# Kernel tuning notes

Hardware: AMD Instinct MI355X
Metric: run time of the kernel (lower is better)

Reference implementation:

```python
import jax, jax.numpy as jnp
import numpy as np

EPS = 1e-5

def gelu(x):
    return jax.nn.gelu(x, approximate=False)

def conv1x1(x, w, b):
    # x: [B,C,H,W], w: [O,C], b: [O]
    return jnp.einsum('bchw,oc->bohw', x, w) + b[None, :, None, None]

def dwconv3(x, w, b):
    # depthwise 3x3, w: [C,1,3,3]
    C = x.shape[1]
    y = jax.lax.conv_general_dilated(x, w, (1, 1), 'SAME',
                                     feature_group_count=C,
                                     dimension_numbers=('NCHW', 'OIHW', 'NCHW'))
    return y + b[None, :, None, None]

def groupnorm(x, g, b):
    # GroupNorm(1, C): normalize over (C,H,W) per sample, per-channel affine
    m = x.mean(axis=(1, 2, 3), keepdims=True)
    v = x.var(axis=(1, 2, 3), keepdims=True)
    xn = (x - m) * jax.lax.rsqrt(v + EPS)
    return xn * g[None, :, None, None] + b[None, :, None, None]

@jax.custom_vjp
def spike(u):
    return (u > 0.0).astype(u.dtype)

def _spike_fwd(u):
    return spike(u), u

def _spike_bwd(u, g):
    # rectangular surrogate gradient of width 0.5 around the threshold
    return (g * (jnp.abs(u) < 0.5).astype(g.dtype),)

spike.defvjp(_spike_fwd, _spike_bwd)

def lif_along(x, tau, vth, axis):
    # leaky-integrate-fire recurrence along `axis` (H or W) treated as time
    xt = jnp.moveaxis(x, axis, 0)  # [T, ...]
    z = jnp.zeros_like(xt[0])
    def step(carry, x_t):
        u_prev, o_prev = carry
        u = x_t + tau * u_prev * (1.0 - o_prev)  # hard reset on spike
        o = spike(u - vth)
        return (u, o), o
    _, out = jax.lax.scan(step, (z, z), xt)
    return jnp.moveaxis(out, 0, axis)


def setup_inputs() -> dict:
    key = jax.random.key(0)
    ks = jax.random.split(key, 8)
    B, C, H, W = 64, 96, 56, 56
    Hd = 4 * C
    def w(k, shape, s=0.02):
        return jax.random.normal(k, shape, jnp.float32) * s
    f32 = jnp.float32
    return dict(
        x=jax.random.normal(ks[0], (B, C, H, W), f32),
        n1g=jnp.ones(C, f32), n1b=jnp.zeros(C, f32),
        c1w=w(ks[1], (C, C)), c1b=jnp.zeros(C, f32),
        g1g=jnp.ones(C, f32), g1b=jnp.zeros(C, f32),
        dww=w(ks[2], (C, 1, 3, 3)), dwb=jnp.zeros(C, f32),
        g2g=jnp.ones(C, f32), g2b=jnp.zeros(C, f32),
        tau1=jnp.array(0.25, f32), vth1=jnp.array(-1.0, f32),
        tau2=jnp.array(0.25, f32), vth2=jnp.array(-1.0, f32),
        c21w=w(ks[3], (C, C)), c21b=jnp.zeros(C, f32),
        c22w=w(ks[4], (C, C)), c22b=jnp.zeros(C, f32),
        g3g=jnp.ones(C, f32), g3b=jnp.zeros(C, f32),
        c3w=w(ks[5], (C, C)), c3b=jnp.zeros(C, f32),
        n2g=jnp.ones(C, f32), n2b=jnp.zeros(C, f32),
        f1w=w(ks[6], (Hd, C)), f1b=jnp.zeros(Hd, f32),
        f2w=w(ks[7], (C, Hd)), f2b=jnp.zeros(C, f32),
    )


def reference(x, n1g, n1b, c1w, c1b, g1g, g1b, dww, dwb, g2g, g2b,
              tau1, vth1, tau2, vth2, c21w, c21b, c22w, c22b,
              g3g, g3b, c3w, c3b, n2g, n2b, f1w, f1b, f2w, f2b):
    shortcut = x
    # LIF module
    h = groupnorm(x, n1g, n1b)                               # block norm1 (MyNorm)
    h = gelu(groupnorm(conv1x1(h, c1w, c1b), g1g, g1b))      # conv1 -> norm1 -> GELU
    h = gelu(groupnorm(dwconv3(h, dww, dwb), g2g, g2b))      # dw1 -> norm2 -> GELU
    x_lr = lif_along(h, tau1, vth1, axis=2)                  # LIF over H
    x_td = lif_along(h, tau2, vth2, axis=3)                  # LIF over W
    h = gelu(conv1x1(x_lr, c21w, c21b)) + gelu(conv1x1(x_td, c22w, c22b))
    h = conv1x1(groupnorm(h, g3g, g3b), c3w, c3b)            # norm3 -> conv3
    x = shortcut + h
    # MLP branch (1x1 convs)
    m = groupnorm(x, n2g, n2b)
    m = conv1x1(gelu(conv1x1(m, f1w, f1b)), f2w, f2b)
    return x + m
```

## Files before the change

### kernel.cpp

```cpp
#include <hip/hip_runtime.h>

#define BB 64
#define CC 96
#define HH 56
#define WW 56
#define HWSZ (HH*WW)
#define CHW (CC*HWSZ)
#define NTOT ((size_t)BB*CHW)
#define S_SPLIT 32
#define CHUNK (CHW/S_SPLIT)
#define HD 384
#define NP 104

typedef float f32x4  __attribute__((ext_vector_type(4)));
typedef short bf16x8 __attribute__((ext_vector_type(8)));
typedef unsigned short u16x4 __attribute__((ext_vector_type(4)));

__device__ __forceinline__ unsigned short f2bf(float f) {
    unsigned int u = __float_as_uint(f);
    u = (u + 0x7FFFu + ((u >> 16) & 1u)) >> 16;
    return (unsigned short)u;
}
__device__ __forceinline__ unsigned int cvtpk(float lo, float hi) {
    unsigned int r;
    asm("v_cvt_pk_bf16_f32 %0, %1, %2" : "=v"(r) : "v"(lo), "v"(hi));
    return r;
}
__device__ __forceinline__ unsigned short cvt1(float x) {
    return (unsigned short)cvtpk(x, x);
}
__device__ __forceinline__ float bf2f(unsigned short u) {
    return __uint_as_float(((unsigned int)u) << 16);
}
__device__ __forceinline__ float gelu_t(float x) {
    float s = x*x;
    float q = __builtin_fmaf(s, 0.102943f, 2.3021953f) * x;
    float t = exp2f(q);
    float r = __builtin_amdgcn_rcpf(1.0f + t);
    return __builtin_fmaf(-x, r, x);
}
__device__ __forceinline__ bf16x8 ldfrag(const unsigned short* p) {
    return *reinterpret_cast<const bf16x8*>(p);
}
template<int NPART>
__device__ __forceinline__ float2 stats_from_parts(const float2* __restrict__ part, int b) {
    int lane = threadIdx.x & 63;
    float s = 0.f, q = 0.f;
    for (int i = lane; i < NPART; i += 64) {
        float2 v = part[b*NPART + i];
        s += v.x; q += v.y;
    }
    #pragma unroll
    for (int off = 32; off > 0; off >>= 1) {
        s += __shfl_down(s, off);
        q += __shfl_down(q, off);
    }
    s = __shfl(s, 0); q = __shfl(q, 0);
    float mean = s / (float)CHW;
    float var  = q / (float)CHW - mean*mean;
    return make_float2(mean, rsqrtf(var + 1e-5f));
}

__global__ __launch_bounds__(256) void wconv(const float* __restrict__ c1w, const float* __restrict__ c21w,
        const float* __restrict__ c22w, const float* __restrict__ c3w,
        const float* __restrict__ f1w, const float* __restrict__ f2w,
        unsigned short* __restrict__ wbf) {
    int i = blockIdx.x*256 + threadIdx.x;
    int blk = i / 9216;
    int idx = i - blk*9216;
    int tm   = idx / 1536;
    int rem  = idx - tm*1536;
    int ks   = rem / 512;
    int rem2 = rem - ks*512;
    int lane = rem2 >> 3;
    int j    = rem2 & 7;
    int row = tm*16 + (lane & 15);
    int col = ks*32 + (lane >> 4)*8 + j;
    float v;
    if      (blk == 0) v = c1w [row*CC + col];
    else if (blk == 1) v = c21w[row*CC + col];
    else if (blk == 2) v = c22w[row*CC + col];
    else if (blk == 3) v = c3w [row*CC + col];
    else if (blk <  8) v = f1w[((blk-4)*CC + row)*CC + col];
    else               v = f2w[row*HD + (blk-8)*CC + col];
    wbf[i] = f2bf(v);
}

__global__ __launch_bounds__(256) void gn_partial(const float* __restrict__ in, float2* __restrict__ part) {
    int b = blockIdx.y, s = blockIdx.x;
    const float4* p = (const float4*)(in + (size_t)b*CHW + (size_t)s*CHUNK);
    float sum = 0.f, sq = 0.f;
    for (int i = threadIdx.x; i < CHUNK/4; i += 256) {
        float4 v = p[i];
        sum += v.x+v.y+v.z+v.w;
        sq  += v.x*v.x+v.y*v.y+v.z*v.z+v.w*v.w;
    }
    #pragma unroll
    for (int off = 32; off > 0; off >>= 1) {
        sum += __shfl_down(sum, off);
        sq  += __shfl_down(sq,  off);
    }
    __shared__ float2 red[4];
    int wid = threadIdx.x >> 6, lane = threadIdx.x & 63;
    if (lane == 0) red[wid] = make_float2(sum, sq);
    __syncthreads();
    if (threadIdx.x == 0) {
        for (int i = 1; i < 4; i++) { sum += red[i].x; sq += red[i].y; }
        part[b*S_SPLIT + s] = make_float2(sum, sq);
    }
}

template<bool IN_BF, bool OUT_RES, int NPART>
__global__ __launch_bounds__(256) void convk(const void* __restrict__ in_,
        const unsigned short* __restrict__ wbf, const float* __restrict__ bias,
        const float2* __restrict__ part_in, const float* __restrict__ gam, const float* __restrict__ bet,
        const float* __restrict__ res, void* __restrict__ out_, float2* __restrict__ part_out) {
    __shared__ unsigned short xs[128][NP];
    __shared__ float af0[CC], bf0[CC], af1[CC], bf1[CC];
    __shared__ float2 red[4];
    int tid = threadIdx.x;
    int b0 = blockIdx.y, b1 = b0 + 32;
    int hw0 = blockIdx.x * 64;
    int lane = tid & 63, wv = tid >> 6;
    int mh = wv >> 1, cg = wv & 1;
    bf16x8 wfr[9];
    {
        const unsigned short* wl = wbf + mh*4608 + lane*8;
        #pragma unroll
        for (int i = 0; i < 9; i++) wfr[i] = ldfrag(wl + i*512);
    }
    float2 st0 = stats_from_parts<NPART>(part_in, b0);
    float2 st1 = stats_from_parts<NPART>(part_in, b1);
    if (tid < CC) {
        float a0 = st0.y * gam[tid];
        af0[tid] = a0; bf0[tid] = __builtin_fmaf(-st0.x, a0, bet[tid]);
        float a1 = st1.y * gam[tid];
        af1[tid] = a1; bf1[tid] = __builtin_fmaf(-st1.x, a1, bet[tid]);
    }
    __syncthreads();
    if (IN_BF) {
        const unsigned short* inb = (const unsigned short*)in_;
        int colp = (tid & 31) * 2;
        for (int c4 = (tid >> 5)*4; c4 < CC; c4 += 32) {
            float v0[4][2], v1[4][2];
            #pragma unroll
            for (int j = 0; j < 4; j++) {
                int c = c4 + j;
                unsigned int u0 = *reinterpret_cast<const unsigned int*>(inb + (size_t)b0*CHW + (size_t)c*HWSZ + hw0 + colp);
                unsigned int u1 = *reinterpret_cast<const unsigned int*>(inb + (size_t)b1*CHW + (size_t)c*HWSZ + hw0 + colp);
                v0[j][0] = __builtin_fmaf(bf2f((unsigned short)u0),        af0[c], bf0[c]);
                v0[j][1] = __builtin_fmaf(bf2f((unsigned short)(u0>>16)),  af0[c], bf0[c]);
                v1[j][0] = __builtin_fmaf(bf2f((unsigned short)u1),        af1[c], bf1[c]);
                v1[j][1] = __builtin_fmaf(bf2f((unsigned short)(u1>>16)),  af1[c], bf1[c]);
            }
            *reinterpret_cast<uint2*>(&xs[colp][c4])      = make_uint2(cvtpk(v0[0][0],v0[1][0]), cvtpk(v0[2][0],v0[3][0]));
            *reinterpret_cast<uint2*>(&xs[colp+1][c4])    = make_uint2(cvtpk(v0[0][1],v0[1][1]), cvtpk(v0[2][1],v0[3][1]));
            *reinterpret_cast<uint2*>(&xs[64+colp][c4])   = make_uint2(cvtpk(v1[0][0],v1[1][0]), cvtpk(v1[2][0],v1[3][0]));
            *reinterpret_cast<uint2*>(&xs[64+colp+1][c4]) = make_uint2(cvtpk(v1[0][1],v1[1][1]), cvtpk(v1[2][1],v1[3][1]));
        }
    } else {
        int col = tid & 63;
        for (int c4 = (tid >> 6)*4; c4 < CC; c4 += 16) {
            float v0[4], v1[4];
            #pragma unroll
            for (int j = 0; j < 4; j++) {
                int c = c4 + j;
                size_t off0 = (size_t)b0*CHW + (size_t)c*HWSZ + hw0 + col;
                size_t off1 = (size_t)b1*CHW + (size_t)c*HWSZ + hw0 + col;
                float r0 = ((const float*)in_)[off0];
                float r1 = ((const float*)in_)[off1];
                v0[j] = __builtin_fmaf(r0, af0[c], bf0[c]);
                v1[j] = __builtin_fmaf(r1, af1[c], bf1[c]);
            }
            *reinterpret_cast<uint2*>(&xs[col][c4])    = make_uint2(cvtpk(v0[0],v0[1]), cvtpk(v0[2],v0[3]));
            *reinterpret_cast<uint2*>(&xs[64+col][c4]) = make_uint2(cvtpk(v1[0],v1[1]), cvtpk(v1[2],v1[3]));
        }
    }
    __syncthreads();
    int ln = lane & 15, k0 = (lane >> 4)*8, r0i = (lane >> 4)*4;
    f32x4 acc[3][4];
    #pragma unroll
    for (int t = 0; t < 3; t++)
        #pragma unroll
        for (int x = 0; x < 4; x++) acc[t][x] = (f32x4){0,0,0,0};
    __builtin_amdgcn_s_setprio(1);
    #pragma unroll
    for (int ks = 0; ks < 3; ks++) {
        bf16x8 bfr[4];
        #pragma unroll
        for (int xr = 0; xr < 4; xr++) bfr[xr] = ldfrag(&xs[cg*64 + xr*16 + ln][ks*32+k0]);
        #pragma unroll
        for (int tm = 0; tm < 3; tm++) {
            #pragma unroll
            for (int xr = 0; xr < 4; xr++)
                acc[tm][xr] = __builtin_amdgcn_mfma_f32_16x16x32_bf16(wfr[tm*3+ks], bfr[xr], acc[tm][xr], 0, 0, 0);
        }
    }
    __builtin_amdgcn_s_setprio(0);
    size_t obase = (size_t)(cg ? b1 : b0)*CHW + hw0;
    float s = 0.f, q = 0.f;
    #pragma unroll
    for (int tm = 0; tm < 3; tm++) {
        #pragma unroll
        for (int xr = 0; xr < 4; xr++) {
            #pragma unroll
            for (int r = 0; r < 4; r++) {
                int o = mh*48 + tm*16 + r0i + r;
                size_t idx = obase + (size_t)o*HWSZ + xr*16 + ln;
                float v = acc[tm][xr][r] + bias[o];
                if (OUT_RES) { v += res[idx]; ((float*)out_)[idx] = v; }
                else         { ((unsigned short*)out_)[idx] = cvt1(v); }
                s += v; q += v*v;
            }
        }
    }
    #pragma unroll
    for (int off = 32; off > 0; off >>= 1) { s += __shfl_down(s, off); q += __shfl_down(q, off); }
    if (lane == 0) red[wv] = make_float2(s, q);
    __syncthreads();
    if (tid == 0) {
        part_out[b0*49 + blockIdx.x] = make_float2(red[0].x + red[2].x, red[0].y + red[2].y);
        part_out[b1*49 + blockIdx.x] = make_float2(red[1].x + red[3].x, red[1].y + red[3].y);
    }
}

__global__ __launch_bounds__(256) void dw_fused(const unsigned short* __restrict__ t1,
        const float* __restrict__ dww, const float* __restrict__ dwb,
        const float2* __restrict__ part_in, const float* __restrict__ gam, const float* __restrict__ bet,
        unsigned short* __restrict__ t2, float2* __restrict__ part_out) {
    __shared__ float tile[HH*57];
    __shared__ float2 red[4];
    int bc = blockIdx.x;
    int b = bc / CC, c = bc - b*CC;
    int tid = threadIdx.x;
    float2 st = stats_from_parts<49>(part_in, b);
    float ga = gam[c]*st.y;
    float bb = __builtin_fmaf(-st.x, ga, bet[c]);
    const unsigned short* ip = t1 + (size_t)bc*HWSZ;
    for (int i = tid; i < HWSZ/4; i += 256) {
        u16x4 v = *reinterpret_cast<const u16x4*>(ip + (size_t)i*4);
        int h = i / 14;
        int w0 = (i - h*14)*4;
        float* tp = &tile[h*57 + w0];
        #pragma unroll
        for (int j = 0; j < 4; j++)
            tp[j] = gelu_t(__builtin_fmaf(bf2f((unsigned short)v[j]), ga, bb));
    }
    __syncthreads();
    float w00=dww[c*9+0],w01=dww[c*9+1],w02=dww[c*9+2],
          w10=dww[c*9+3],w11=dww[c*9+4],w12=dww[c*9+5],
          w20=dww[c*9+6],w21=dww[c*9+7],w22=dww[c*9+8];
    float bs = dwb[c];
    unsigned short* op = t2 + (size_t)bc*HWSZ;
    float s = 0.f, q = 0.f;
    for (int i = tid; i < HWSZ; i += 256) {
        int h = i/WW, w_ = i - h*WW;
        float acc = bs;
        int up = h > 0, dn = h < HH-1, lf = w_ > 0, rt = w_ < WW-1;
        const float* rm = &tile[(h-1)*57 + w_];
        const float* r0p = &tile[h*57 + w_];
        const float* rp = &tile[(h+1)*57 + w_];
        if (up) { if (lf) acc += rm[-1]*w00; acc += rm[0]*w01; if (rt) acc += rm[1]*w02; }
        if (lf) acc += r0p[-1]*w10;
        acc += r0p[0]*w11;
        if (rt) acc += r0p[1]*w12;
        if (dn) { if (lf) acc += rp[-1]*w20; acc += rp[0]*w21; if (rt) acc += rp[1]*w22; }
        op[i] = cvt1(acc);
        s += acc; q += acc*acc;
    }
    #pragma unroll
    for (int off = 32; off > 0; off >>= 1) { s += __shfl_down(s, off); q += __shfl_down(q, off); }
    int wid = tid >> 6, lane = tid & 63;
    if (lane == 0) red[wid] = make_float2(s, q);
    __syncthreads();
    if (tid == 0) {
        for (int i = 1; i < 4; i++) { s += red[i].x; q += red[i].y; }
        part_out[bc] = make_float2(s, q);
    }
}

__global__ __launch_bounds__(64) void lif_hw(const unsigned short* __restrict__ t2,
        unsigned short* __restrict__ xlr, unsigned short* __restrict__ xtd,
        const float2* __restrict__ part_in, const float* __restrict__ gam, const float* __restrict__ bet,
        const float* __restrict__ tau1p, const float* __restrict__ vth1p,
        const float* __restrict__ tau2p, const float* __restrict__ vth2p) {
    __shared__ unsigned short tile[HH*58];
    int bc = blockIdx.x;
    int b = bc / CC, c = bc - b*CC;
    int tid = threadIdx.x;
    float2 st = stats_from_parts<96>(part_in, b);
    float ga = gam[c]*st.y;
    float bb = __builtin_fmaf(-st.x, ga, bet[c]);
    const unsigned short* ip = t2 + (size_t)bc*HWSZ;
    for (int i = tid; i < HWSZ/4; i += 64) {
        u16x4 v = *reinterpret_cast<const u16x4*>(ip + i*4);
        int h = i / 14;
        int w0 = (i - h*14)*4;
        unsigned short* tp = &tile[h*58 + w0];
        #pragma unroll
        for (int j = 0; j < 4; j++)
            tp[j] = cvt1(gelu_t(__builtin_fmaf(bf2f((unsigned short)v[j]), ga, bb)));
    }
    __syncthreads();
    const float tau1 = *tau1p, vth1 = *vth1p;
    if (tid < WW) {
        float u = 0.f, o = 0.f;
        unsigned short* op = xlr + (size_t)bc*HWSZ + tid;
        for (int h = 0; h < HH; h++) {
            float xv = bf2f(tile[h*58 + tid]);
            u = xv + tau1*u*(1.f - o);
            o = (u - vth1 > 0.f) ? 1.f : 0.f;
            op[h*WW] = (o != 0.f) ? (unsigned short)0x3F80 : (unsigned short)0;
        }
    }
    __syncthreads();
    const float tau2 = *tau2p, vth2 = *vth2p;
    if (tid < HH) {
        float u = 0.f, o = 0.f;
        int off = tid*58;
        for (int w_ = 0; w_ < WW; w_++) {
            float xv = bf2f(tile[off + w_]);
            u = xv + tau2*u*(1.f - o);
            o = (u - vth2 > 0.f) ? 1.f : 0.f;
            tile[off + w_] = (o != 0.f) ? (unsigned short)0x3F80 : (unsigned short)0;
        }
    }
    __syncthreads();
    unsigned int* op32 = (unsigned int*)(xtd + (size_t)bc*HWSZ);
    for (int i = tid; i < HWSZ/2; i += 64) {
        int h = i / 28;
        int w0 = (i - h*28)*2;
        op32[i] = (unsigned int)tile[h*58 + w0] | ((unsigned int)tile[h*58 + w0 + 1] << 16);
    }
}

__global__ __launch_bounds__(256) void dual_mfma(const unsigned short* __restrict__ xa_g, const unsigned short* __restrict__ xb_g,
        const unsigned short* __restrict__ w1bf, const float* __restrict__ b1,
        const unsigned short* __restrict__ w2bf, const float* __restrict__ b2,
        unsigned short* __restrict__ out, float2* __restrict__ part_out) {
    __shared__ unsigned short xa[64][NP];
    __shared__ unsigned short xb[64][NP];
    __shared__ float2 red[4];
    int tid = threadIdx.x;
    int b = blockIdx.y;
    int hw0 = blockIdx.x * 64;
    {
        int colp = (tid & 31) * 2;
        const unsigned short* ap = xa_g + (size_t)b*CHW + hw0 + colp;
        const unsigned short* bp = xb_g + (size_t)b*CHW + hw0 + colp;
        for (int c4 = (tid >> 5)*4; c4 < CC; c4 += 32) {
            unsigned int ua[4], ub[4];
            #pragma unroll
            for (int j = 0; j < 4; j++) {
                ua[j] = *reinterpret_cast<const unsigned int*>(ap + (size_t)(c4+j)*HWSZ);
                ub[j] = *reinterpret_cast<const unsigned int*>(bp + (size_t)(c4+j)*HWSZ);
            }
            *reinterpret_cast<uint2*>(&xa[colp][c4]) =
                make_uint2((ua[0]&0xFFFFu)|(ua[1]<<16), (ua[2]&0xFFFFu)|(ua[3]<<16));
            *reinterpret_cast<uint2*>(&xa[colp+1][c4]) =
                make_uint2((ua[0]>>16)|(ua[1]&0xFFFF0000u), (ua[2]>>16)|(ua[3]&0xFFFF0000u));
            *reinterpret_cast<uint2*>(&xb[colp][c4]) =
                make_uint2((ub[0]&0xFFFFu)|(ub[1]<<16), (ub[2]&0xFFFFu)|(ub[3]<<16));
            *reinterpret_cast<uint2*>(&xb[colp+1][c4]) =
                make_uint2((ub[0]>>16)|(ub[1]&0xFFFF0000u), (ub[2]>>16)|(ub[3]&0xFFFF0000u));
        }
    }
    __syncthreads();
    int lane = tid & 63, wv = tid >> 6;
    int mh = wv >> 1, cg = wv & 1;
    int ln = lane & 15, k0 = (lane >> 4)*8, r0i = (lane >> 4)*4;
    const unsigned short* wl1 = w1bf + mh*4608 + lane*8;
    const unsigned short* wl2 = w2bf + mh*4608 + lane*8;
    f32x4 acc1[3][2], acc2[3][2];
    #pragma unroll
    for (int t = 0; t < 3; t++) {
        acc1[t][0] = (f32x4){0,0,0,0}; acc1[t][1] = (f32x4){0,0,0,0};
        acc2[t][0] = (f32x4){0,0,0,0}; acc2[t][1] = (f32x4){0,0,0,0};
    }
    __builtin_amdgcn_s_setprio(1);
    #pragma unroll
    for (int ks = 0; ks < 3; ks++) {
        bf16x8 bfa0 = ldfrag(&xa[cg*32 + ln][ks*32+k0]);
        bf16x8 bfa1 = ldfrag(&xa[cg*32 + 16 + ln][ks*32+k0]);
        bf16x8 bfb0 = ldfrag(&xb[cg*32 + ln][ks*32+k0]);
        bf16x8 bfb1 = ldfrag(&xb[cg*32 + 16 + ln][ks*32+k0]);
        #pragma unroll
        for (int tm = 0; tm < 3; tm++) {
            bf16x8 af1 = ldfrag(wl1 + (tm*3+ks)*512);
            bf16x8 af2 = ldfrag(wl2 + (tm*3+ks)*512);
            acc1[tm][0] = __builtin_amdgcn_mfma_f32_16x16x32_bf16(af1, bfa0, acc1[tm][0], 0, 0, 0);
            acc1[tm][1] = __builtin_amdgcn_mfma_f32_16x16x32_bf16(af1, bfa1, acc1[tm][1], 0, 0, 0);
            acc2[tm][0] = __builtin_amdgcn_mfma_f32_16x16x32_bf16(af2, bfb0, acc2[tm][0], 0, 0, 0);
            acc2[tm][1] = __builtin_amdgcn_mfma_f32_16x16x32_bf16(af2, bfb1, acc2[tm][1], 0, 0, 0);
        }
    }
    __builtin_amdgcn_s_setprio(0);
    size_t ob = (size_t)b*CHW + hw0;
    float s = 0.f, q = 0.f;
    #pragma unroll
    for (int tm = 0; tm < 3; tm++) {
        #pragma unroll
        for (int xr = 0; xr < 2; xr++) {
            #pragma unroll
            for (int r = 0; r < 4; r++) {
                int o = mh*48 + tm*16 + r0i + r;
                float v = gelu_t(acc1[tm][xr][r] + b1[o]) + gelu_t(acc2[tm][xr][r] + b2[o]);
                out[ob + (size_t)o*HWSZ + cg*32 + xr*16 + ln] = cvt1(v);
                s += v; q += v*v;
            }
        }
    }
    #pragma unroll
    for (int off = 32; off > 0; off >>= 1) { s += __shfl_down(s, off); q += __shfl_down(q, off); }
    if (lane == 0) red[wv] = make_float2(s, q);
    __syncthreads();
    if (tid == 0) {
        for (int i = 1; i < 4; i++) { s += red[i].x; q += red[i].y; }
        part_out[b*49 + blockIdx.x] = make_float2(s, q);
    }
}

__global__ __launch_bounds__(512, 4) void mlp_mfma(float* __restrict__ xio, const float2* __restrict__ part_in,
        const float* __restrict__ gam, const float* __restrict__ bet,
        const unsigned short* __restrict__ wbf, const float* __restrict__ b1, const float* __restrict__ b2) {
    __shared__ unsigned short xs[128][NP];
    __shared__ unsigned short mc[128][NP];
    __shared__ float afc[2][CC], bfc[2][CC];
    int tid = threadIdx.x;
    int b0 = blockIdx.y, b1i = b0 + 32;
    int hw0 = blockIdx.x * 64;
    int lane = tid & 63, wv = tid >> 6;
    int mh = wv >> 2;
    int cg = wv & 3;
    float2 st0 = stats_from_parts<49>(part_in, b0);
    float2 st1 = stats_from_parts<49>(part_in, b1i);
    if (tid < CC) {
        float a0 = st0.y * gam[tid];
        afc[0][tid] = a0; bfc[0][tid] = __builtin_fmaf(-st0.x, a0, bet[tid]);
        float a1 = st1.y * gam[tid];
        afc[1][tid] = a1; bfc[1][tid] = __builtin_fmaf(-st1.x, a1, bet[tid]);
    }
    __syncthreads();
    {
        int col = tid & 63;
        int bsel0 = (tid >> 6) & 1;
        size_t base = (size_t)(bsel0 ? b1i : b0)*CHW + hw0 + col;
        for (int c4 = (tid >> 7)*4; c4 < CC; c4 += 16) {
            float v[4];
            #pragma unroll
            for (int j = 0; j < 4; j++) {
                int c = c4 + j;
                float rv = xio[base + (size_t)c*HWSZ];
                v[j] = __builtin_fmaf(rv, afc[bsel0][c], bfc[bsel0][c]);
            }
            *reinterpret_cast<uint2*>(&xs[bsel0*64 + col][c4]) =
                make_uint2(cvtpk(v[0],v[1]), cvtpk(v[2],v[3]));
        }
    }
    __syncthreads();
    int ln = lane & 15, k0 = (lane >> 4)*8;
    int r0i = (lane >> 4)*4;
    int xrow0 = cg*32 + ln;
    int xrow1 = xrow0 + 16;
    int bsel = cg >> 1;
    size_t ob = (size_t)(bsel ? b1i : b0)*CHW + hw0 + (cg & 1)*32 + ln;
    float xv0[3][4], xv1[3][4];
    #pragma unroll
    for (int tm = 0; tm < 3; tm++) {
        #pragma unroll
        for (int r = 0; r < 4; r++) {
            size_t i0 = ob + (size_t)(mh*48 + tm*16 + r0i + r)*HWSZ;
            xv0[tm][r] = xio[i0];
            xv1[tm][r] = xio[i0 + 16];
        }
    }
    f32x4 ao[3][2];
    #pragma unroll
    for (int t = 0; t < 3; t++) { ao[t][0] = (f32x4){0,0,0,0}; ao[t][1] = (f32x4){0,0,0,0}; }
    for (int ch = 0; ch < 4; ch++) {
        const unsigned short* w1l = wbf + (4+ch)*9216 + mh*4608 + lane*8;
        const unsigned short* w2l = wbf + (8+ch)*9216 + mh*4608 + lane*8;
        f32x4 c1[3][2];
        #pragma unroll
        for (int t = 0; t < 3; t++) { c1[t][0] = (f32x4){0,0,0,0}; c1[t][1] = (f32x4){0,0,0,0}; }
        __builtin_amdgcn_s_setprio(1);
        #pragma unroll
        for (int ks = 0; ks < 3; ks++) {
            bf16x8 bfa = ldfrag(&xs[xrow0][ks*32+k0]);
            bf16x8 bfb = ldfrag(&xs[xrow1][ks*32+k0]);
            #pragma unroll
            for (int tm = 0; tm < 3; tm++) {
                bf16x8 af = ldfrag(w1l + (tm*3+ks)*512);
                c1[tm][0] = __builtin_amdgcn_mfma_f32_16x16x32_bf16(af, bfa, c1[tm][0], 0, 0, 0);
                c1[tm][1] = __builtin_amdgcn_mfma_f32_16x16x32_bf16(af, bfb, c1[tm][1], 0, 0, 0);
            }
        }
        __builtin_amdgcn_s_setprio(0);
        #pragma unroll
        for (int tm = 0; tm < 3; tm++) {
            int d0 = mh*48 + tm*16 + r0i;
            int dch = ch*CC + d0;
            float g0 = gelu_t(c1[tm][0][0] + b1[dch+0]);
            float g1 = gelu_t(c1[tm][0][1] + b1[dch+1]);
            float g2 = gelu_t(c1[tm][0][2] + b1[dch+2]);
            float g3 = gelu_t(c1[tm][0][3] + b1[dch+3]);
            *reinterpret_cast<uint2*>(&mc[xrow0][d0]) = make_uint2(cvtpk(g0,g1), cvtpk(g2,g3));
            float h0 = gelu_t(c1[tm][1][0] + b1[dch+0]);
            float h1 = gelu_t(c1[tm][1][1] + b1[dch+1]);
            float h2 = gelu_t(c1[tm][1][2] + b1[dch+2]);
            float h3 = gelu_t(c1[tm][1][3] + b1[dch+3]);
            *reinterpret_cast<uint2*>(&mc[xrow1][d0]) = make_uint2(cvtpk(h0,h1), cvtpk(h2,h3));
        }
        __syncthreads();
        __builtin_amdgcn_s_setprio(1);
        #pragma unroll
        for (int ks = 0; ks < 3; ks++) {
            bf16x8 bfa = ldfrag(&mc[xrow0][ks*32+k0]);
            bf16x8 bfb = ldfrag(&mc[xrow1][ks*32+k0]);
            #pragma unroll
            for (int tm = 0; tm < 3; tm++) {
                bf16x8 af = ldfrag(w2l + (tm*3+ks)*512);
                ao[tm][0] = __builtin_amdgcn_mfma_f32_16x16x32_bf16(af, bfa, ao[tm][0], 0, 0, 0);
                ao[tm][1] = __builtin_amdgcn_mfma_f32_16x16x32_bf16(af, bfb, ao[tm][1], 0, 0, 0);
            }
        }
        __builtin_amdgcn_s_setprio(0);
        __syncthreads();
    }
    #pragma unroll
    for (int tm = 0; tm < 3; tm++) {
        #pragma unroll
        for (int r = 0; r < 4; r++) {
            int o = mh*48 + tm*16 + r0i + r;
            size_t i0 = ob + (size_t)o*HWSZ;
            float bo = b2[o];
            xio[i0]      = xv0[tm][r] + bo + ao[tm][0][r];
            xio[i0 + 16] = xv1[tm][r] + bo + ao[tm][1][r];
        }
    }
}

extern "C" void kernel_launch(void* const* d_in, const int* in_sizes, int n_in,
                              void* d_out, int out_size, void* d_ws, size_t ws_size,
                              hipStream_t stream) {
    (void)in_sizes; (void)n_in; (void)out_size; (void)ws_size;
    const float* x    = (const float*)d_in[0];
    const float* n1g  = (const float*)d_in[1];
    const float* n1b  = (const float*)d_in[2];
    const float* c1w  = (const float*)d_in[3];
    const float* c1b  = (const float*)d_in[4];
    const float* g1g  = (const float*)d_in[5];
    const float* g1b  = (const float*)d_in[6];
    const float* dww  = (const float*)d_in[7];
    const float* dwb  = (const float*)d_in[8];
    const float* g2g  = (const float*)d_in[9];
    const float* g2b  = (const float*)d_in[10];
    const float* tau1 = (const float*)d_in[11];
    const float* vth1 = (const float*)d_in[12];
    const float* tau2 = (const float*)d_in[13];
    const float* vth2 = (const float*)d_in[14];
    const float* c21w = (const float*)d_in[15];
    const float* c21b = (const float*)d_in[16];
    const float* c22w = (const float*)d_in[17];
    const float* c22b = (const float*)d_in[18];
    const float* g3g  = (const float*)d_in[19];
    const float* g3b  = (const float*)d_in[20];
    const float* c3w  = (const float*)d_in[21];
    const float* c3b  = (const float*)d_in[22];
    const float* n2g  = (const float*)d_in[23];
    const float* n2b  = (const float*)d_in[24];
    const float* f1w  = (const float*)d_in[25];
    const float* f1b  = (const float*)d_in[26];
    const float* f2w  = (const float*)d_in[27];
    const float* f2b  = (const float*)d_in[28];
    float* out = (float*)d_out;

    unsigned short* A   = (unsigned short*)d_ws;
    unsigned short* Bb  = A  + NTOT;
    unsigned short* Cc  = Bb + NTOT;
    unsigned short* WBF = Cc + NTOT;
    float2* part0 = (float2*)(WBF + 110592);
    float2* part1 = part0 + 64*32;
    float2* part2 = part1 + 64*49;
    float2* part3 = part2 + 64*96;
    float2* part4 = part3 + 64*49;

    const unsigned short* Wc1  = WBF;
    const unsigned short* Wc21 = WBF + 9216;
    const unsigned short* Wc22 = WBF + 18432;
    const unsigned short* Wc3  = WBF + 27648;

    dim3 gStat(S_SPLIT, BB);
    dim3 gPair(HWSZ/64, BB/2);
    dim3 gSing(HWSZ/64, BB);

    wconv<<<432,256,0,stream>>>(c1w, c21w, c22w, c3w, f1w, f2w, WBF);
    gn_partial<<<gStat,256,0,stream>>>(x, part0);
    convk<false,false,S_SPLIT><<<gPair,256,0,stream>>>(x, Wc1, c1b, part0, n1g, n1b, nullptr, A, part1);
    dw_fused<<<BB*CC,256,0,stream>>>(A, dww, dwb, part1, g1g, g1b, Bb, part2);
    lif_hw<<<BB*CC,64,0,stream>>>(Bb, A, Cc, part2, g2g, g2b, tau1, vth1, tau2, vth2);
    dual_mfma<<<gSing,256,0,stream>>>(A, Cc, Wc21, c21b, Wc22, c22b, Bb, part3);
    convk<true,true,49><<<gPair,256,0,stream>>>(Bb, Wc3, c3b, part3, g3g, g3b, x, out, part4);
    mlp_mfma<<<gPair,512,0,stream>>>(out, part4, n2g, n2b, WBF, f1b, f2b);
}
```

Baseline: 293.1 us.

## Store LIF spike maps as bytes and widen fp32 input loads

The LIF kernel now writes both spike maps as one byte per element instead of bf16, using an extra shared byte tile for the H-direction spikes. dual_mfma reads these bytes and expands them to bf16 1.0/0.0 while staging into LDS. This halves the traffic of the two intermediate spike tensors. In addition, the fp32 path of convk now uses float2 vector loads through the same loop as the bf16 path. The residual read in mlp_mfma is moved from before the GEMMs to the final store, which lowers register pressure but puts that load latency at the end.

```diff
diff --git a/kernel.cpp b/kernel.cpp
--- a/kernel.cpp
+++ b/kernel.cpp
@@ -138,42 +138,35 @@
         af1[tid] = a1; bf1[tid] = __builtin_fmaf(-st1.x, a1, bet[tid]);
     }
     __syncthreads();
-    if (IN_BF) {
-        const unsigned short* inb = (const unsigned short*)in_;
+    {
         int colp = (tid & 31) * 2;
         for (int c4 = (tid >> 5)*4; c4 < CC; c4 += 32) {
             float v0[4][2], v1[4][2];
             #pragma unroll
             for (int j = 0; j < 4; j++) {
                 int c = c4 + j;
-                unsigned int u0 = *reinterpret_cast<const unsigned int*>(inb + (size_t)b0*CHW + (size_t)c*HWSZ + hw0 + colp);
-                unsigned int u1 = *reinterpret_cast<const unsigned int*>(inb + (size_t)b1*CHW + (size_t)c*HWSZ + hw0 + colp);
-                v0[j][0] = __builtin_fmaf(bf2f((unsigned short)u0),        af0[c], bf0[c]);
-                v0[j][1] = __builtin_fmaf(bf2f((unsigned short)(u0>>16)),  af0[c], bf0[c]);
-                v1[j][0] = __builtin_fmaf(bf2f((unsigned short)u1),        af1[c], bf1[c]);
-                v1[j][1] = __builtin_fmaf(bf2f((unsigned short)(u1>>16)),  af1[c], bf1[c]);
+                size_t off0 = (size_t)b0*CHW + (size_t)c*HWSZ + hw0 + colp;
+                size_t off1 = (size_t)b1*CHW + (size_t)c*HWSZ + hw0 + colp;
+                float r00, r01, r10, r11;
+                if (IN_BF) {
+                    unsigned int u0 = *reinterpret_cast<const unsigned int*>((const unsigned short*)in_ + off0);
+                    unsigned int u1 = *reinterpret_cast<const unsigned int*>((const unsigned short*)in_ + off1);
+                    r00 = bf2f((unsigned short)u0); r01 = bf2f((unsigned short)(u0>>16));
+                    r10 = bf2f((unsigned short)u1); r11 = bf2f((unsigned short)(u1>>16));
+                } else {
+                    float2 f0 = *reinterpret_cast<const float2*>((const float*)in_ + off0);
+                    float2 f1 = *reinterpret_cast<const float2*>((const float*)in_ + off1);
+                    r00 = f0.x; r01 = f0.y; r10 = f1.x; r11 = f1.y;
+                }
+                v0[j][0] = __builtin_fmaf(r00, af0[c], bf0[c]);
+                v0[j][1] = __builtin_fmaf(r01, af0[c], bf0[c]);
+                v1[j][0] = __builtin_fmaf(r10, af1[c], bf1[c]);
+                v1[j][1] = __builtin_fmaf(r11, af1[c], bf1[c]);
             }
             *reinterpret_cast<uint2*>(&xs[colp][c4])      = make_uint2(cvtpk(v0[0][0],v0[1][0]), cvtpk(v0[2][0],v0[3][0]));
             *reinterpret_cast<uint2*>(&xs[colp+1][c4])    = make_uint2(cvtpk(v0[0][1],v0[1][1]), cvtpk(v0[2][1],v0[3][1]));
             *reinterpret_cast<uint2*>(&xs[64+colp][c4])   = make_uint2(cvtpk(v1[0][0],v1[1][0]), cvtpk(v1[2][0],v1[3][0]));
             *reinterpret_cast<uint2*>(&xs[64+colp+1][c4]) = make_uint2(cvtpk(v1[0][1],v1[1][1]), cvtpk(v1[2][1],v1[3][1]));
-        }
-    } else {
-        int col = tid & 63;
-        for (int c4 = (tid >> 6)*4; c4 < CC; c4 += 16) {
-            float v0[4], v1[4];
-            #pragma unroll
-            for (int j = 0; j < 4; j++) {
-                int c = c4 + j;
-                size_t off0 = (size_t)b0*CHW + (size_t)c*HWSZ + hw0 + col;
-                size_t off1 = (size_t)b1*CHW + (size_t)c*HWSZ + hw0 + col;
-                float r0 = ((const float*)in_)[off0];
-                float r1 = ((const float*)in_)[off1];
-                v0[j] = __builtin_fmaf(r0, af0[c], bf0[c]);
-                v1[j] = __builtin_fmaf(r1, af1[c], bf1[c]);
-            }
-            *reinterpret_cast<uint2*>(&xs[col][c4])    = make_uint2(cvtpk(v0[0],v0[1]), cvtpk(v0[2],v0[3]));
-            *reinterpret_cast<uint2*>(&xs[64+col][c4]) = make_uint2(cvtpk(v1[0],v1[1]), cvtpk(v1[2],v1[3]));
         }
     }
     __syncthreads();
@@ -280,11 +273,12 @@
 }
 
 __global__ __launch_bounds__(64) void lif_hw(const unsigned short* __restrict__ t2,
-        unsigned short* __restrict__ xlr, unsigned short* __restrict__ xtd,
+        unsigned char* __restrict__ xlr, unsigned char* __restrict__ xtd,
         const float2* __restrict__ part_in, const float* __restrict__ gam, const float* __restrict__ bet,
         const float* __restrict__ tau1p, const float* __restrict__ vth1p,
         const float* __restrict__ tau2p, const float* __restrict__ vth2p) {
     __shared__ unsigned short tile[HH*58];
+    __shared__ unsigned char spA[HH*60];
     int bc = blockIdx.x;
     int b = bc / CC, c = bc - b*CC;
     int tid = threadIdx.x;
@@ -305,12 +299,11 @@
     const float tau1 = *tau1p, vth1 = *vth1p;
     if (tid < WW) {
         float u = 0.f, o = 0.f;
-        unsigned short* op = xlr + (size_t)bc*HWSZ + tid;
         for (int h = 0; h < HH; h++) {
             float xv = bf2f(tile[h*58 + tid]);
             u = xv + tau1*u*(1.f - o);
             o = (u - vth1 > 0.f) ? 1.f : 0.f;
-            op[h*WW] = (o != 0.f) ? (unsigned short)0x3F80 : (unsigned short)0;
+            spA[h*60 + tid] = (o != 0.f) ? 1 : 0;
         }
     }
     __syncthreads();
@@ -322,19 +315,26 @@
             float xv = bf2f(tile[off + w_]);
             u = xv + tau2*u*(1.f - o);
             o = (u - vth2 > 0.f) ? 1.f : 0.f;
-            tile[off + w_] = (o != 0.f) ? (unsigned short)0x3F80 : (unsigned short)0;
-        }
-    }
-    __syncthreads();
-    unsigned int* op32 = (unsigned int*)(xtd + (size_t)bc*HWSZ);
-    for (int i = tid; i < HWSZ/2; i += 64) {
-        int h = i / 28;
-        int w0 = (i - h*28)*2;
-        op32[i] = (unsigned int)tile[h*58 + w0] | ((unsigned int)tile[h*58 + w0 + 1] << 16);
-    }
-}
-
-__global__ __launch_bounds__(256) void dual_mfma(const unsigned short* __restrict__ xa_g, const unsigned short* __restrict__ xb_g,
+            tile[off + w_] = (o != 0.f) ? 1 : 0;
+        }
+    }
+    __syncthreads();
+    size_t base = (size_t)bc*HWSZ;
+    unsigned int* lr32 = (unsigned int*)(xlr + base);
+    unsigned int* td32 = (unsigned int*)(xtd + base);
+    for (int i = tid; i < HWSZ/4; i += 64) {
+        int h = i / 14;
+        int w0 = (i - h*14)*4;
+        unsigned int a = (unsigned int)spA[h*60+w0] | ((unsigned int)spA[h*60+w0+1]<<8)
+                       | ((unsigned int)spA[h*60+w0+2]<<16) | ((unsigned int)spA[h*60+w0+3]<<24);
+        unsigned int t = (unsigned int)(tile[h*58+w0]&1) | ((unsigned int)(tile[h*58+w0+1]&1)<<8)
+                       | ((unsigned int)(tile[h*58+w0+2]&1)<<16) | ((unsigned int)(tile[h*58+w0+3]&1)<<24);
+        lr32[i] = a;
+        td32[i] = t;
+    }
+}
+
+__global__ __launch_bounds__(256) void dual_mfma(const unsigned char* __restrict__ xa_g, const unsigned char* __restrict__ xb_g,
         const unsigned short* __restrict__ w1bf, const float* __restrict__ b1,
         const unsigned short* __restrict__ w2bf, const float* __restrict__ b2,
         unsigned short* __restrict__ out, float2* __restrict__ part_out) {
@@ -345,24 +345,26 @@
     int b = blockIdx.y;
     int hw0 = blockIdx.x * 64;
     {
-        int colp = (tid & 31) * 2;
-        const unsigned short* ap = xa_g + (size_t)b*CHW + hw0 + colp;
-        const unsigned short* bp = xb_g + (size_t)b*CHW + hw0 + colp;
-        for (int c4 = (tid >> 5)*4; c4 < CC; c4 += 32) {
+        int colq = (tid & 15) * 4;
+        const unsigned char* ap = xa_g + (size_t)b*CHW + hw0 + colq;
+        const unsigned char* bp = xb_g + (size_t)b*CHW + hw0 + colq;
+        for (int c4 = (tid >> 4)*4; c4 < CC; c4 += 64) {
             unsigned int ua[4], ub[4];
             #pragma unroll
             for (int j = 0; j < 4; j++) {
                 ua[j] = *reinterpret_cast<const unsigned int*>(ap + (size_t)(c4+j)*HWSZ);
                 ub[j] = *reinterpret_cast<const unsigned int*>(bp + (size_t)(c4+j)*HWSZ);
             }
-            *reinterpret_cast<uint2*>(&xa[colp][c4]) =
-                make_uint2((ua[0]&0xFFFFu)|(ua[1]<<16), (ua[2]&0xFFFFu)|(ua[3]<<16));
-            *reinterpret_cast<uint2*>(&xa[colp+1][c4]) =
-                make_uint2((ua[0]>>16)|(ua[1]&0xFFFF0000u), (ua[2]>>16)|(ua[3]&0xFFFF0000u));
-            *reinterpret_cast<uint2*>(&xb[colp][c4]) =
-                make_uint2((ub[0]&0xFFFFu)|(ub[1]<<16), (ub[2]&0xFFFFu)|(ub[3]<<16));
-            *reinterpret_cast<uint2*>(&xb[colp+1][c4]) =
-                make_uint2((ub[0]>>16)|(ub[1]&0xFFFF0000u), (ub[2]>>16)|(ub[3]&0xFFFF0000u));
+            #pragma unroll
+            for (int jj = 0; jj < 4; jj++) {
+                unsigned int sh = jj*8;
+                unsigned int la = (((ua[0]>>sh)&1u)*0x3F80u) | (((ua[1]>>sh)&1u)*0x3F800000u);
+                unsigned int ha = (((ua[2]>>sh)&1u)*0x3F80u) | (((ua[3]>>sh)&1u)*0x3F800000u);
+                unsigned int lb = (((ub[0]>>sh)&1u)*0x3F80u) | (((ub[1]>>sh)&1u)*0x3F800000u);
+                unsigned int hb = (((ub[2]>>sh)&1u)*0x3F80u) | (((ub[3]>>sh)&1u)*0x3F800000u);
+                *reinterpret_cast<uint2*>(&xa[colq+jj][c4]) = make_uint2(la, ha);
+                *reinterpret_cast<uint2*>(&xb[colq+jj][c4]) = make_uint2(lb, hb);
+            }
         }
     }
     __syncthreads();
@@ -462,18 +464,6 @@
     int r0i = (lane >> 4)*4;
     int xrow0 = cg*32 + ln;
     int xrow1 = xrow0 + 16;
-    int bsel = cg >> 1;
-    size_t ob = (size_t)(bsel ? b1i : b0)*CHW + hw0 + (cg & 1)*32 + ln;
-    float xv0[3][4], xv1[3][4];
-    #pragma unroll
-    for (int tm = 0; tm < 3; tm++) {
-        #pragma unroll
-        for (int r = 0; r < 4; r++) {
-            size_t i0 = ob + (size_t)(mh*48 + tm*16 + r0i + r)*HWSZ;
-            xv0[tm][r] = xio[i0];
-            xv1[tm][r] = xio[i0 + 16];
-        }
-    }
     f32x4 ao[3][2];
     #pragma unroll
     for (int t = 0; t < 3; t++) { ao[t][0] = (f32x4){0,0,0,0}; ao[t][1] = (f32x4){0,0,0,0}; }
@@ -527,6 +517,8 @@
         __builtin_amdgcn_s_setprio(0);
         __syncthreads();
     }
+    int bsel = cg >> 1;
+    size_t ob = (size_t)(bsel ? b1i : b0)*CHW + hw0 + (cg & 1)*32 + ln;
     #pragma unroll
     for (int tm = 0; tm < 3; tm++) {
         #pragma unroll
@@ -534,8 +526,8 @@
             int o = mh*48 + tm*16 + r0i + r;
             size_t i0 = ob + (size_t)o*HWSZ;
             float bo = b2[o];
-            xio[i0]      = xv0[tm][r] + bo + ao[tm][0][r];
-            xio[i0 + 16] = xv1[tm][r] + bo + ao[tm][1][r];
+            xio[i0]      = xio[i0]      + bo + ao[tm][0][r];
+            xio[i0 + 16] = xio[i0 + 16] + bo + ao[tm][1][r];
         }
     }
 }
@@ -590,6 +582,9 @@
     const unsigned short* Wc22 = WBF + 18432;
     const unsigned short* Wc3  = WBF + 27648;
 
+    unsigned char* Au8 = (unsigned char*)A;
+    unsigned char* Cu8 = (unsigned char*)Cc;
+
     dim3 gStat(S_SPLIT, BB);
     dim3 gPair(HWSZ/64, BB/2);
     dim3 gSing(HWSZ/64, BB);
@@ -598,8 +593,8 @@
     gn_partial<<<gStat,256,0,stream>>>(x, part0);
     convk<false,false,S_SPLIT><<<gPair,256,0,stream>>>(x, Wc1, c1b, part0, n1g, n1b, nullptr, A, part1);
     dw_fused<<<BB*CC,256,0,stream>>>(A, dww, dwb, part1, g1g, g1b, Bb, part2);
-    lif_hw<<<BB*CC,64,0,stream>>>(Bb, A, Cc, part2, g2g, g2b, tau1, vth1, tau2, vth2);
-    dual_mfma<<<gSing,256,0,stream>>>(A, Cc, Wc21, c21b, Wc22, c22b, Bb, part3);
+    lif_hw<<<BB*CC,64,0,stream>>>(Bb, Au8, Cu8, part2, g2g, g2b, tau1, vth1, tau2, vth2);
+    dual_mfma<<<gSing,256,0,stream>>>(Au8, Cu8, Wc21, c21b, Wc22, c22b, Bb, part3);
     convk<true,true,49><<<gPair,256,0,stream>>>(Bb, Wc3, c3b, part3, g3g, g3b, x, out, part4);
     mlp_mfma<<<gPair,512,0,stream>>>(out, part4, n2g, n2b, WBF, f1b, f2b);
 }
```

After: 289.2 us. No clear change (-1.3%).
